# Performance work log

Hardware: AMD Instinct MI355X
Metric: run time of the kernel (lower is better)

The kernel has to match this reference:

```python
import jax, jax.numpy as jnp
import numpy as np

E = 128  # embedding_dim
H = 128  # hidden_dim


def setup_inputs() -> dict:
    key = jax.random.key(0)
    ks = jax.random.split(key, 8)
    B, N = 64, 20000
    s = 1.0 / np.sqrt(E)
    return {
        "session_repr": jax.random.normal(ks[0], (B, E), jnp.float32),
        "target_embeddings": jax.random.normal(ks[1], (N, E), jnp.float32),
        "W1": jax.random.uniform(ks[2], (E, H), jnp.float32, -s, s),
        "b1": jax.random.uniform(ks[3], (H,), jnp.float32, -s, s),
        "W2": jax.random.uniform(ks[4], (E, H), jnp.float32, -s, s),
        "b2": jax.random.uniform(ks[5], (H,), jnp.float32, -s, s),
        "W3": jax.random.uniform(ks[6], (H, 1), jnp.float32, -1.0 / np.sqrt(H), 1.0 / np.sqrt(H)),
        "b3": jax.random.uniform(ks[7], (1,), jnp.float32, -1.0 / np.sqrt(H), 1.0 / np.sqrt(H)),
    }


def reference(session_repr, target_embeddings, W1, b1, W2, b2, W3, b3):
    # Project once, then broadcast-add (same math as projecting expanded tensors).
    sp = session_repr @ W1 + b1            # [B, H]
    tp = target_embeddings @ W2 + b2       # [N, H]
    h = jnp.tanh(sp[:, None, :] + tp[None, :, :])  # [B, N, H]
    # Dropout is identity in eval mode.
    scores = jnp.einsum('bnh,ho->bn', h, W3) + b3[0]  # [B, N]
    return scores
```

## Files before the change

### kernel.cpp

```cpp
#include <hip/hip_runtime.h>

#define BSES 64
#define EDIM 128
#define HDIM 128
#define NT 40
#define KSCALE 2.8853900817779268f

typedef float v2f __attribute__((ext_vector_type(2)));

__device__ __forceinline__ float fexp2(float x) {
#if __has_builtin(__builtin_amdgcn_exp2f)
  return __builtin_amdgcn_exp2f(x);
#else
  return exp2f(x);
#endif
}
__device__ __forceinline__ float frcp(float x) {
#if __has_builtin(__builtin_amdgcn_rcpf)
  return __builtin_amdgcn_rcpf(x);
#else
  return 1.0f / x;
#endif
}
__device__ __forceinline__ v2f mkv2(float a, float b) {
  v2f r;
  r.x = a;
  r.y = b;
  return r;
}

__device__ __forceinline__ float g4pk8(float4 s0, float4 s1, float4 w0,
                                       float4 w1, float4 v0, float4 v1,
                                       float acc) {
  const v2f one = {1.f, 1.f};
  v2f s01 = mkv2(s0.x, s0.y), s23 = mkv2(s0.z, s0.w);
  v2f s45 = mkv2(s1.x, s1.y), s67 = mkv2(s1.z, s1.w);
  v2f w01 = mkv2(w0.x, w0.y), w23 = mkv2(w0.z, w0.w);
  v2f w45 = mkv2(w1.x, w1.y), w67 = mkv2(w1.z, w1.w);
  v2f v01 = mkv2(v0.x, v0.y), v23 = mkv2(v0.z, v0.w);
  v2f v45 = mkv2(v1.x, v1.y), v67 = mkv2(v1.z, v1.w);
  v2f x01 = __builtin_elementwise_fma(s01, v01, one);
  v2f x23 = __builtin_elementwise_fma(s23, v23, one);
  v2f x45 = __builtin_elementwise_fma(s45, v45, one);
  v2f x67 = __builtin_elementwise_fma(s67, v67, one);
  v2f p03 = x01 * x23;
  v2f p47 = x45 * x67;
  v2f n03 = __builtin_elementwise_fma(w23, x01, w01 * x23);
  v2f n47 = __builtin_elementwise_fma(w67, x45, w45 * x67);
  v2f num = __builtin_elementwise_fma(n47, p03, n03 * p47);
  v2f den = p03 * p47;
  acc = fmaf(num.x, frcp(den.x), acc);
  acc = fmaf(num.y, frcp(den.y), acc);
  return acc;
}

__global__ __launch_bounds__(256) void taa_esp(
    const float* __restrict__ sess, const float* __restrict__ W1,
    const float* __restrict__ b1, const float* __restrict__ W3,
    const float* __restrict__ b3, float* __restrict__ esp4,
    float* __restrict__ C_out) {
  int t = blockIdx.x * 256 + threadIdx.x;
  if (t < BSES * HDIM) {
    int b = t >> 7, h = t & 127;
    const float* srow = sess + b * EDIM;
    float acc = 0.f;
#pragma unroll 4
    for (int e = 0; e < EDIM; ++e)
      acc = fmaf(srow[e], W1[e * HDIM + h], acc);
    esp4[(h >> 2) * 256 + b * 4 + (h & 3)] = fexp2((acc + b1[h]) * KSCALE);
  }
  if (t == 0) {
    float s = b3[0];
    for (int i = 0; i < HDIM; ++i) s += W3[i];
    *C_out = s;
  }
}

__device__ __forceinline__ void score5x2(
    const float* __restrict__ et, int t0, int sp2,
    const float* __restrict__ esp4, const float* __restrict__ w3,
    float accA[5], float accB[5]) {
  const float* base = et + t0 * HDIM;
#pragma unroll 2
  for (int c = 0; c < 8; ++c) {
    float4 spA[4], spB[4];
#pragma unroll
    for (int k = 0; k < 4; ++k) {
      const float* p = esp4 + ((c << 2) + k) * 256 + (sp2 << 3);
      spA[k] = *(const float4*)p;
      spB[k] = *(const float4*)(p + 4);
    }
    float4 wq[4];
#pragma unroll
    for (int k = 0; k < 4; ++k)
      wq[k] = *(const float4*)(w3 + (c << 4) + k * 4);
#pragma unroll
    for (int t = 0; t < 5; ++t) {
      const float* rp = base + t * HDIM + (c << 4);
      float4 v0 = *(const float4*)(rp + 0);
      float4 v1 = *(const float4*)(rp + 4);
      float4 v2 = *(const float4*)(rp + 8);
      float4 v3 = *(const float4*)(rp + 12);
      accA[t] = g4pk8(spA[0], spA[1], wq[0], wq[1], v0, v1, accA[t]);
      accA[t] = g4pk8(spA[2], spA[3], wq[2], wq[3], v2, v3, accA[t]);
      accB[t] = g4pk8(spB[0], spB[1], wq[0], wq[1], v0, v1, accB[t]);
      accB[t] = g4pk8(spB[2], spB[3], wq[2], wq[3], v2, v3, accB[t]);
    }
  }
}

__global__ __launch_bounds__(256) void taa_fused(
    const float* __restrict__ emb, const float* __restrict__ W2,
    const float* __restrict__ b2, const float* __restrict__ esp4,
    const float* __restrict__ w3, const float* __restrict__ Cptr,
    float* __restrict__ out, int N) {
  __shared__ float sm[NT][132];
  __shared__ float et[NT * HDIM];
  const int nb = blockIdx.x * NT;

  for (int k = threadIdx.x; k < NT * 32; k += 256) {
    int r = k >> 5, c4 = k & 31;
    float4 v = make_float4(0.f, 0.f, 0.f, 0.f);
    if (nb + r < N) v = ((const float4*)(emb + (size_t)(nb + r) * EDIM))[c4];
    *(float4*)&sm[r][c4 * 4] = v;
  }
  __syncthreads();

  {
    const int h4 = (threadIdx.x & 31) * 4;
    const int rg = threadIdx.x >> 5;
    float acc[5][4];
#pragma unroll
    for (int j = 0; j < 5; ++j)
#pragma unroll
      for (int q = 0; q < 4; ++q) acc[j][q] = 0.f;
    for (int e = 0; e < EDIM; e += 4) {
      float4 w[4];
#pragma unroll
      for (int q = 0; q < 4; ++q)
        w[q] = *(const float4*)(W2 + (size_t)(e + q) * HDIM + h4);
#pragma unroll
      for (int j = 0; j < 5; ++j) {
        float4 em = *(const float4*)&sm[rg * 5 + j][e];
        acc[j][0] = fmaf(em.x, w[0].x, acc[j][0]);
        acc[j][1] = fmaf(em.x, w[0].y, acc[j][1]);
        acc[j][2] = fmaf(em.x, w[0].z, acc[j][2]);
        acc[j][3] = fmaf(em.x, w[0].w, acc[j][3]);
        acc[j][0] = fmaf(em.y, w[1].x, acc[j][0]);
        acc[j][1] = fmaf(em.y, w[1].y, acc[j][1]);
        acc[j][2] = fmaf(em.y, w[1].z, acc[j][2]);
        acc[j][3] = fmaf(em.y, w[1].w, acc[j][3]);
        acc[j][0] = fmaf(em.z, w[2].x, acc[j][0]);
        acc[j][1] = fmaf(em.z, w[2].y, acc[j][1]);
        acc[j][2] = fmaf(em.z, w[2].z, acc[j][2]);
        acc[j][3] = fmaf(em.z, w[2].w, acc[j][3]);
        acc[j][0] = fmaf(em.w, w[3].x, acc[j][0]);
        acc[j][1] = fmaf(em.w, w[3].y, acc[j][1]);
        acc[j][2] = fmaf(em.w, w[3].z, acc[j][2]);
        acc[j][3] = fmaf(em.w, w[3].w, acc[j][3]);
      }
    }
    float4 bb2 = *(const float4*)(b2 + h4);
#pragma unroll
    for (int j = 0; j < 5; ++j) {
      int nr = rg * 5 + j;
      float4 o;
      o.x = fexp2((acc[j][0] + bb2.x) * KSCALE);
      o.y = fexp2((acc[j][1] + bb2.y) * KSCALE);
      o.z = fexp2((acc[j][2] + bb2.z) * KSCALE);
      o.w = fexp2((acc[j][3] + bb2.w) * KSCALE);
      *(float4*)&et[nr * HDIM + h4] = o;
    }
  }
  __syncthreads();

  const int lane = threadIdx.x & 63;
  const int wv = threadIdx.x >> 6;
  const int sp2 = lane & 31;
  const int th = lane >> 5;
  const int t0 = (wv * 2 + th) * 5;
  float accA[5] = {0.f, 0.f, 0.f, 0.f, 0.f};
  float accB[5] = {0.f, 0.f, 0.f, 0.f, 0.f};
  score5x2(et, t0, sp2, esp4, w3, accA, accB);

  const float Cv = *Cptr;
  const int n0 = nb + t0;
  const int sA = sp2 * 2, sB = sA + 1;
  float* poA = out + (size_t)sA * N + n0;
  float* poB = out + (size_t)sB * N + n0;
#pragma unroll
  for (int t = 0; t < 5; ++t) {
    if (n0 + t < N) {
      poA[t] = fmaf(-2.f, accA[t], Cv);
      poB[t] = fmaf(-2.f, accB[t], Cv);
    }
  }
}

extern "C" void kernel_launch(void* const* d_in, const int* in_sizes, int n_in,
                              void* d_out, int out_size, void* d_ws, size_t ws_size,
                              hipStream_t stream) {
  const float* sess = (const float*)d_in[0];
  const float* emb  = (const float*)d_in[1];
  const float* W1   = (const float*)d_in[2];
  const float* b1   = (const float*)d_in[3];
  const float* W2   = (const float*)d_in[4];
  const float* b2   = (const float*)d_in[5];
  const float* W3   = (const float*)d_in[6];
  const float* b3   = (const float*)d_in[7];
  float* out = (float*)d_out;
  const int B = in_sizes[0] / EDIM;
  const int N = in_sizes[1] / EDIM;

  float* esp4 = (float*)d_ws;
  float* Cp   = esp4 + (size_t)BSES * HDIM;

  taa_esp<<<(B * HDIM + 255) / 256, 256, 0, stream>>>(sess, W1, b1, W3, b3,
                                                      esp4, Cp);
  taa_fused<<<(N + NT - 1) / NT, 256, 0, stream>>>(emb, W2, b2, esp4, W3, Cp,
                                                   out, N);
}
```

Measured before the change: 39.52 us.

## Compute target projection with bf16 MFMA using a pre-swizzled W2

Replaces the per-block fp32 FMA target projection (emb @ W2) with bf16 16x16x32 MFMA instructions. W2 is converted once to bf16 in the prologue kernel and laid out in MFMA fragment order, and embedding tiles are converted to bf16 fragments in LDS. The et tile stride is padded to 132 to reduce bank conflicts in the scoring loop. In exchange, the projection now runs at bf16 input precision, which adds rounding error before the exp/tanh stage.

```diff
diff --git a/kernel.cpp b/kernel.cpp
--- a/kernel.cpp
+++ b/kernel.cpp
@@ -4,9 +4,12 @@
 #define EDIM 128
 #define HDIM 128
 #define NT 40
+#define ETS 132
 #define KSCALE 2.8853900817779268f
 
 typedef float v2f __attribute__((ext_vector_type(2)));
+typedef __attribute__((ext_vector_type(8))) short short8;
+typedef __attribute__((ext_vector_type(4))) float f32x4;
 
 __device__ __forceinline__ float fexp2(float x) {
 #if __has_builtin(__builtin_amdgcn_exp2f)
@@ -27,6 +30,10 @@
   r.x = a;
   r.y = b;
   return r;
+}
+__device__ __forceinline__ unsigned short f2bf(float f) {
+  unsigned int u = __float_as_uint(f);
+  return (unsigned short)((u + 0x7FFFu + ((u >> 16) & 1u)) >> 16);
 }
 
 __device__ __forceinline__ float g4pk8(float4 s0, float4 s1, float4 w0,
@@ -56,9 +63,10 @@
 
 __global__ __launch_bounds__(256) void taa_esp(
     const float* __restrict__ sess, const float* __restrict__ W1,
-    const float* __restrict__ b1, const float* __restrict__ W3,
-    const float* __restrict__ b3, float* __restrict__ esp4,
-    float* __restrict__ C_out) {
+    const float* __restrict__ b1, const float* __restrict__ W2,
+    const float* __restrict__ W3, const float* __restrict__ b3,
+    float* __restrict__ esp4, float* __restrict__ C_out,
+    unsigned short* __restrict__ w2f) {
   int t = blockIdx.x * 256 + threadIdx.x;
   if (t < BSES * HDIM) {
     int b = t >> 7, h = t & 127;
@@ -69,6 +77,17 @@
       acc = fmaf(srow[e], W1[e * HDIM + h], acc);
     esp4[(h >> 2) * 256 + b * 4 + (h & 3)] = fexp2((acc + b1[h]) * KSCALE);
   }
+#pragma unroll
+  for (int rep = 0; rep < 2; ++rep) {
+    int idx = t + rep * 8192;
+    int j = idx & 7;
+    int l = (idx >> 3) & 63;
+    int ks = (idx >> 9) & 3;
+    int nt = (idx >> 11) & 7;
+    int k = ks * 32 + ((l >> 4) << 3) + j;
+    int n = nt * 16 + (l & 15);
+    w2f[idx] = f2bf(W2[k * HDIM + n]);
+  }
   if (t == 0) {
     float s = b3[0];
     for (int i = 0; i < HDIM; ++i) s += W3[i];
@@ -80,7 +99,7 @@
     const float* __restrict__ et, int t0, int sp2,
     const float* __restrict__ esp4, const float* __restrict__ w3,
     float accA[5], float accB[5]) {
-  const float* base = et + t0 * HDIM;
+  const float* base = et + t0 * ETS;
 #pragma unroll 2
   for (int c = 0; c < 8; ++c) {
     float4 spA[4], spB[4];
@@ -96,7 +115,7 @@
       wq[k] = *(const float4*)(w3 + (c << 4) + k * 4);
 #pragma unroll
     for (int t = 0; t < 5; ++t) {
-      const float* rp = base + t * HDIM + (c << 4);
+      const float* rp = base + t * ETS + (c << 4);
       float4 v0 = *(const float4*)(rp + 0);
       float4 v1 = *(const float4*)(rp + 4);
       float4 v2 = *(const float4*)(rp + 8);
@@ -110,74 +129,79 @@
 }
 
 __global__ __launch_bounds__(256) void taa_fused(
-    const float* __restrict__ emb, const float* __restrict__ W2,
+    const float* __restrict__ emb, const unsigned short* __restrict__ w2f,
     const float* __restrict__ b2, const float* __restrict__ esp4,
     const float* __restrict__ w3, const float* __restrict__ Cptr,
     float* __restrict__ out, int N) {
-  __shared__ float sm[NT][132];
-  __shared__ float et[NT * HDIM];
+  __shared__ short ebf[12 * 512];
+  __shared__ float et[NT * ETS];
+  const int tid = threadIdx.x;
+  const int l = tid & 63;
+  const int wv = tid >> 6;
   const int nb = blockIdx.x * NT;
 
-  for (int k = threadIdx.x; k < NT * 32; k += 256) {
-    int r = k >> 5, c4 = k & 31;
-    float4 v = make_float4(0.f, 0.f, 0.f, 0.f);
-    if (nb + r < N) v = ((const float4*)(emb + (size_t)(nb + r) * EDIM))[c4];
-    *(float4*)&sm[r][c4 * 4] = v;
+#pragma unroll
+  for (int pi = 0; pi < 3; ++pi) {
+    const int p = wv + pi * 4;
+    const int mt = p >> 2, ks = p & 3;
+    int row = nb + mt * 16 + (l & 15);
+    row = min(row, N - 1);
+    const int k0 = ks * 32 + ((l >> 4) << 3);
+    const float4 f0 = *(const float4*)(emb + (size_t)row * EDIM + k0);
+    const float4 f1 = *(const float4*)(emb + (size_t)row * EDIM + k0 + 4);
+    short8 v;
+    v[0] = (short)f2bf(f0.x);
+    v[1] = (short)f2bf(f0.y);
+    v[2] = (short)f2bf(f0.z);
+    v[3] = (short)f2bf(f0.w);
+    v[4] = (short)f2bf(f1.x);
+    v[5] = (short)f2bf(f1.y);
+    v[6] = (short)f2bf(f1.z);
+    v[7] = (short)f2bf(f1.w);
+    *(short8*)&ebf[(p << 9) + (l << 3)] = v;
   }
   __syncthreads();
 
   {
-    const int h4 = (threadIdx.x & 31) * 4;
-    const int rg = threadIdx.x >> 5;
-    float acc[5][4];
-#pragma unroll
-    for (int j = 0; j < 5; ++j)
-#pragma unroll
-      for (int q = 0; q < 4; ++q) acc[j][q] = 0.f;
-    for (int e = 0; e < EDIM; e += 4) {
-      float4 w[4];
-#pragma unroll
-      for (int q = 0; q < 4; ++q)
-        w[q] = *(const float4*)(W2 + (size_t)(e + q) * HDIM + h4);
-#pragma unroll
-      for (int j = 0; j < 5; ++j) {
-        float4 em = *(const float4*)&sm[rg * 5 + j][e];
-        acc[j][0] = fmaf(em.x, w[0].x, acc[j][0]);
-        acc[j][1] = fmaf(em.x, w[0].y, acc[j][1]);
-        acc[j][2] = fmaf(em.x, w[0].z, acc[j][2]);
-        acc[j][3] = fmaf(em.x, w[0].w, acc[j][3]);
-        acc[j][0] = fmaf(em.y, w[1].x, acc[j][0]);
-        acc[j][1] = fmaf(em.y, w[1].y, acc[j][1]);
-        acc[j][2] = fmaf(em.y, w[1].z, acc[j][2]);
-        acc[j][3] = fmaf(em.y, w[1].w, acc[j][3]);
-        acc[j][0] = fmaf(em.z, w[2].x, acc[j][0]);
-        acc[j][1] = fmaf(em.z, w[2].y, acc[j][1]);
-        acc[j][2] = fmaf(em.z, w[2].z, acc[j][2]);
-        acc[j][3] = fmaf(em.z, w[2].w, acc[j][3]);
-        acc[j][0] = fmaf(em.w, w[3].x, acc[j][0]);
-        acc[j][1] = fmaf(em.w, w[3].y, acc[j][1]);
-        acc[j][2] = fmaf(em.w, w[3].z, acc[j][2]);
-        acc[j][3] = fmaf(em.w, w[3].w, acc[j][3]);
+    const int nt0 = wv * 2;
+    f32x4 acc[3][2];
+#pragma unroll
+    for (int mt = 0; mt < 3; ++mt)
+#pragma unroll
+      for (int j = 0; j < 2; ++j) acc[mt][j] = (f32x4){0.f, 0.f, 0.f, 0.f};
+#pragma unroll
+    for (int ks = 0; ks < 4; ++ks) {
+      short8 a0 = *(short8*)&ebf[((0 * 4 + ks) << 9) + (l << 3)];
+      short8 a1 = *(short8*)&ebf[((1 * 4 + ks) << 9) + (l << 3)];
+      short8 a2 = *(short8*)&ebf[((2 * 4 + ks) << 9) + (l << 3)];
+      short8 b0 = *(const short8*)(w2f + (((nt0 + 0) * 4 + ks) << 9) + (l << 3));
+      short8 b1 = *(const short8*)(w2f + (((nt0 + 1) * 4 + ks) << 9) + (l << 3));
+      acc[0][0] = __builtin_amdgcn_mfma_f32_16x16x32_bf16(a0, b0, acc[0][0], 0, 0, 0);
+      acc[0][1] = __builtin_amdgcn_mfma_f32_16x16x32_bf16(a0, b1, acc[0][1], 0, 0, 0);
+      acc[1][0] = __builtin_amdgcn_mfma_f32_16x16x32_bf16(a1, b0, acc[1][0], 0, 0, 0);
+      acc[1][1] = __builtin_amdgcn_mfma_f32_16x16x32_bf16(a1, b1, acc[1][1], 0, 0, 0);
+      acc[2][0] = __builtin_amdgcn_mfma_f32_16x16x32_bf16(a2, b0, acc[2][0], 0, 0, 0);
+      acc[2][1] = __builtin_amdgcn_mfma_f32_16x16x32_bf16(a2, b1, acc[2][1], 0, 0, 0);
+    }
+    const int nA = nt0 * 16 + (l & 15);
+    const int nB = nA + 16;
+    const float b2A = b2[nA], b2B = b2[nB];
+#pragma unroll
+    for (int mt = 0; mt < 3; ++mt) {
+#pragma unroll
+      for (int r = 0; r < 4; ++r) {
+        const int m = mt * 16 + ((l >> 4) << 2) + r;
+        if (m < NT) {
+          et[m * ETS + nA] = fexp2((acc[mt][0][r] + b2A) * KSCALE);
+          et[m * ETS + nB] = fexp2((acc[mt][1][r] + b2B) * KSCALE);
+        }
       }
     }
-    float4 bb2 = *(const float4*)(b2 + h4);
-#pragma unroll
-    for (int j = 0; j < 5; ++j) {
-      int nr = rg * 5 + j;
-      float4 o;
-      o.x = fexp2((acc[j][0] + bb2.x) * KSCALE);
-      o.y = fexp2((acc[j][1] + bb2.y) * KSCALE);
-      o.z = fexp2((acc[j][2] + bb2.z) * KSCALE);
-      o.w = fexp2((acc[j][3] + bb2.w) * KSCALE);
-      *(float4*)&et[nr * HDIM + h4] = o;
-    }
   }
   __syncthreads();
 
-  const int lane = threadIdx.x & 63;
-  const int wv = threadIdx.x >> 6;
-  const int sp2 = lane & 31;
-  const int th = lane >> 5;
+  const int sp2 = l & 31;
+  const int th = l >> 5;
   const int t0 = (wv * 2 + th) * 5;
   float accA[5] = {0.f, 0.f, 0.f, 0.f, 0.f};
   float accB[5] = {0.f, 0.f, 0.f, 0.f, 0.f};
@@ -214,9 +238,10 @@
 
   float* esp4 = (float*)d_ws;
   float* Cp   = esp4 + (size_t)BSES * HDIM;
-
-  taa_esp<<<(B * HDIM + 255) / 256, 256, 0, stream>>>(sess, W1, b1, W3, b3,
-                                                      esp4, Cp);
-  taa_fused<<<(N + NT - 1) / NT, 256, 0, stream>>>(emb, W2, b2, esp4, W3, Cp,
-                                                   out, N);
-}
+  unsigned short* w2f = (unsigned short*)(Cp + 4);
+
+  taa_esp<<<(B * HDIM + 255) / 256, 256, 0, stream>>>(sess, W1, b1, W2, W3,
+                                                      b3, esp4, Cp, w2f);
+  taa_fused<<<(N + NT - 1) / NT, 256, 0, stream>>>(emb, w2f, b2, esp4, W3,
+                                                   Cp, out, N);
+}
```

Measured after the change: 32.24 us, median of 2. -18.4%, faster.
